# Optimization experiments

Measured on AMD Instinct MI355X. Metric: run time of the kernel, lower is better.

The kernel has to match this reference:

```python
import jax, jax.numpy as jnp
import numpy as np

B, L, S, H = 8, 128, 160, 768      # batch, words, wordpieces, bert hidden
T, CD = 16, 50                      # max chars per word, char embed/lstm dim
WV, WD = 50000, 100                 # word vocab, word embed dim
CV = 128                            # char vocab
NEG = -1e30


def _run_lstm(x, w_ih, w_hh, b):
    # x: [N, T, D] -> hidden states [N, T, Hc]; torch LSTM gate order i,f,g,o
    N = x.shape[0]
    Hc = w_hh.shape[1]
    def step(carry, xt):
        h, c = carry
        g = xt @ w_ih.T + h @ w_hh.T + b
        i, f, gg, o = jnp.split(g, 4, axis=-1)
        c = jax.nn.sigmoid(f) * c + jax.nn.sigmoid(i) * jnp.tanh(gg)
        h = jax.nn.sigmoid(o) * jnp.tanh(c)
        return (h, c), h
    init = (jnp.zeros((N, Hc), x.dtype), jnp.zeros((N, Hc), x.dtype))
    _, hs = jax.lax.scan(step, init, jnp.swapaxes(x, 0, 1))
    return jnp.swapaxes(hs, 0, 1)


def setup_inputs() -> dict:
    key = jax.random.key(0)
    ks = jax.random.split(key, 14)
    sc = 1.0 / np.sqrt(CD)
    return {
        "bert_emb": jax.random.normal(ks[0], (B, S, H), jnp.float32),
        "pieces2word": jax.random.randint(ks[1], (B, L, S), 0, 2, jnp.int32),
        "word_ids": jax.random.randint(ks[2], (B, L), 0, WV),
        "char_ids": jax.random.randint(ks[3], (B, L, T), 0, CV),
        "char_count": jax.random.randint(ks[4], (B, L), 0, T, jnp.int32),
        "token_masks_char": jax.random.randint(ks[5], (B, L, T), 0, 2, jnp.int32),
        "word_table": jax.random.normal(ks[6], (WV, WD), jnp.float32) * 0.02,
        "char_table": jax.random.normal(ks[7], (CV, CD), jnp.float32) * 0.02,
        "w_ih_f": jax.random.uniform(ks[8], (4 * CD, CD), jnp.float32, -sc, sc),
        "w_hh_f": jax.random.uniform(ks[9], (4 * CD, CD), jnp.float32, -sc, sc),
        "b_f": jax.random.uniform(ks[10], (4 * CD,), jnp.float32, -sc, sc),
        "w_ih_b": jax.random.uniform(ks[11], (4 * CD, CD), jnp.float32, -sc, sc),
        "w_hh_b": jax.random.uniform(ks[12], (4 * CD, CD), jnp.float32, -sc, sc),
        "b_b": jax.random.uniform(ks[13], (4 * CD,), jnp.float32, -sc, sc),
    }


def reference(bert_emb, pieces2word, word_ids, char_ids, char_count,
              token_masks_char, word_table, char_table,
              w_ih_f, w_hh_f, b_f, w_ih_b, w_hh_b, b_b):
    cls_embedding = bert_emb[:, 0]                      # [B, H]
    # piece -> word max pooling (masked fill with global min, then max)
    min_value = jax.lax.stop_gradient(jnp.min(bert_emb))
    expanded = jnp.where(pieces2word[:, :, :, None] != 0,
                         bert_emb[:, None, :, :], min_value)  # [B, L, S, H]
    word_reps = jnp.max(expanded, axis=2)               # [B, L, H]

    # word embedding lookup (emb_dropout is identity in eval)
    word_embed = word_table[word_ids]                   # [B, L, WD]

    # char biLSTM
    N = B * L
    lengths = jnp.maximum(char_count.reshape(N), 1)     # char_count[==0] = 1
    x = char_table[char_ids.reshape(N, T)]              # [N, T, CD]
    h_fwd = _run_lstm(x, w_ih_f, w_hh_f, b_f)           # [N, T, CD]
    # reverse each sequence by its true length (packed-sequence semantics)
    t = jnp.arange(T)
    rev_idx = lengths[:, None] - 1 - t[None, :]         # [N, T]
    valid = (rev_idx >= 0).astype(x.dtype)[:, :, None]
    gidx = jnp.clip(rev_idx, 0, T - 1)[:, :, None]
    x_rev = jnp.take_along_axis(x, gidx, axis=1) * valid
    h_rev = _run_lstm(x_rev, w_ih_b, w_hh_b, b_b)
    h_bwd = jnp.take_along_axis(h_rev, gidx, axis=1) * valid  # un-reverse + zero pad
    char_h = jnp.concatenate([h_fwd, h_bwd], axis=-1).reshape(B, L, T, 2 * CD)

    # combine(..., 'max'): additive -1e30 mask, max over chars, zero all-masked
    m = jnp.where(token_masks_char[:, :, :, None] == 0, NEG, 0.0).astype(char_h.dtype)
    h_token_char = jnp.max(m + char_h, axis=2)
    h_token_char = jnp.where(h_token_char == NEG, 0.0, h_token_char)  # [B, L, 2CD]

    embeds = jnp.concatenate([word_reps, word_embed, h_token_char], axis=-1)
    return embeds, cls_embedding
```

## Files before the change

kernel.cpp:

```cpp
#include <hip/hip_runtime.h>

#define B_   8
#define L_   128
#define S_   160
#define H_   768
#define T_   16
#define CD_  50
#define WD_  100
#define NGATE 200
#define NEGV (-1e30f)
#define FMAXV 3.402823466e+38f
#define NELEM (B_ * S_ * H_)

typedef short  s16x8 __attribute__((ext_vector_type(8)));
typedef float  f32x4 __attribute__((ext_vector_type(4)));

#define WL_OFF     0
#define WL_BYTES   (NGATE * 256)
#define XALL_OFF   (WL_OFF + WL_BYTES)
#define XALL_BYTES (T_ * 128 * 16)
#define HBUF_OFF   (XALL_OFF + XALL_BYTES)
#define HBUF_BYTES (2 * 128 * 16)
#define META_OFF   (HBUF_OFF + HBUF_BYTES)
#define SMEM_TOTAL (META_OFF + 32 * 4)

__device__ __forceinline__ unsigned short f2bf(float f) {
    unsigned u = __float_as_uint(f);
    u = (u + 0x7FFFu + ((u >> 16) & 1u)) >> 16;
    return (unsigned short)u;
}
__device__ __forceinline__ float sigm(float x) {
    return __fdividef(1.f, 1.f + __expf(-x));
}
__device__ __forceinline__ float tanh_fast(float x) {
    float a = fabsf(x);
    float e = __expf(-2.f * a);
    float t = __fdividef(1.f - e, 1.f + e);
    return copysignf(t, x);
}
__device__ __forceinline__ float4 fmax4(float4 a, float4 b) {
    return make_float4(fmaxf(a.x, b.x), fmaxf(a.y, b.y), fmaxf(a.z, b.z), fmaxf(a.w, b.w));
}

__device__ void lstm_body(int unit, char* smem,
        const int* __restrict__ char_ids, const int* __restrict__ char_count,
        const int* __restrict__ tok_mask, const float* __restrict__ char_table,
        const float* __restrict__ w_ih_f, const float* __restrict__ w_hh_f,
        const float* __restrict__ b_f,
        const float* __restrict__ w_ih_b, const float* __restrict__ w_hh_b,
        const float* __restrict__ b_b,
        float* __restrict__ out) {
    unsigned short* wl16 = (unsigned short*)(smem + WL_OFF);
    s16x8*          xal  = (s16x8*)(smem + XALL_OFF);
    s16x8*          hb   = (s16x8*)(smem + HBUF_OFF);
    int*            slen = (int*)(smem + META_OFF);
    int*            smask = slen + 16;

    const int dir  = unit >> 6;
    const int grp  = unit & 63;
    const int tid  = threadIdx.x;
    const int lane = tid & 63;
    const int wv   = tid >> 6;

    const float* WI = dir ? w_ih_b : w_ih_f;
    const float* WH = dir ? w_hh_b : w_hh_f;
    const float* BV = dir ? b_b    : b_f;

    if (tid < 16) {
        int n = grp * 16 + tid;
        int c = char_count[n];
        slen[tid] = (c > 0) ? c : 1;
        int mb = 0;
        for (int t = 0; t < T_; ++t) mb |= (tok_mask[n * T_ + t] != 0) << t;
        smask[tid] = mb;
    }
    if (tid < 256) { s16x8 z = {0,0,0,0,0,0,0,0}; hb[tid] = z; }

    for (int idx = tid; idx < NGATE * 16; idx += 512) {
        int r  = idx >> 4;
        int kc = idx & 15;
        int kbase = kc * 8;
        const float* wi = WI + r * CD_;
        const float* wh = WH + r * CD_;
        s16x8 fr = {0,0,0,0,0,0,0,0};
#pragma unroll
        for (int e = 0; e < 8; ++e) {
            int k = kbase + e;
            float v = 0.f;
            if (k < 64) {
                if (k < CD_) v = wi[k];
                else if (k == 63) v = BV[r];
            } else {
                int kk = k - 64;
                if (kk < CD_) v = wh[kk];
            }
            fr[e] = (short)f2bf(v);
        }
        *(s16x8*)((char*)wl16 + r * 256 + ((kc ^ (r & 7)) << 4)) = fr;
    }
    __syncthreads();

    for (int idx = tid; idx < T_ * 128; idx += 512) {
        int t = idx >> 7;
        int u = idx & 127;
        int g = u >> 4, s = u & 15;
        int st = dir ? (slen[s] - 1 - t) : t;
        s16x8 fr = {0,0,0,0,0,0,0,0};
        if (st >= 0) {
            int cidv = char_ids[(grp * 16 + s) * T_ + st];
            const float* row = char_table + cidv * CD_;
            int kbase = g * 8;
#pragma unroll
            for (int e = 0; e < 8; ++e) {
                int k = kbase + e;
                if (k < CD_) fr[e] = (short)f2bf(row[k]);
            }
        }
        if (g == 7) fr[7] = (short)0x3F80;
        xal[t * 128 + u] = fr;
    }

    const int m   = lane & 3;
    const int k2  = (lane >> 2) & 3;
    const int q   = lane >> 4;
    const int sstar = q * 4 + m;

    const int  ntA = wv;
    const int  ntB = 8 + wv;
    const bool hasB = (wv < 5);
    const int  cA = ntA * 4 + k2;
    const int  cB = ntB * 4 + k2;
    const bool vB = hasB && (cB < CD_);
    const int  hofsA = ((cA >> 3) * 16 + sstar) * 8 + (cA & 7);
    const int  hofsB = ((cB >> 3) * 16 + sstar) * 8 + (cB & 7);

    const int orowA = m * 50 + cA;
    const int orowB = m * 50 + ((cB < CD_) ? cB : 0);
#define WADDR(R, KT) ((R) * 256 + (((((KT) << 2) + q) ^ ((R) & 7)) << 4))
    const int baA0 = WADDR(orowA, 0), baA1 = WADDR(orowA, 1);
    const int baA2 = WADDR(orowA, 2), baA3 = WADDR(orowA, 3);
    const int baB0 = WADDR(orowB, 0), baB1 = WADDR(orowB, 1);
    const int baB2 = WADDR(orowB, 2), baB3 = WADDR(orowB, 3);

    const int laneofs = (q << 4) + (lane & 15);
    const int sl_s = slen[sstar];
    const int sm_s = smask[sstar];

    int sms = 0;
#pragma unroll
    for (int t = 0; t < T_; ++t) {
        int tt = dir ? (sl_s - 1 - t) : t;
        if (tt >= 0 && ((sm_s >> tt) & 1)) sms |= 1 << t;
    }

    float cstA = 0.f, cstB = 0.f;
    float mrA = NEGV, mrB = NEGV;
    const bool m0 = (lane & 1) != 0;
    const bool m1 = (lane & 2) != 0;

    __syncthreads();

    const char* wl = (const char*)wl16;

#define TRUPD(VLD, HOF, CST, MR, D) { \
    float v0 = (D)[0], v1 = (D)[1], v2 = (D)[2], v3 = (D)[3]; \
    float s10 = __shfl_xor(v0, 1), s11 = __shfl_xor(v1, 1); \
    float s12 = __shfl_xor(v2, 1), s13 = __shfl_xor(v3, 1); \
    float A0 = m0 ? s11 : v0; \
    float A1 = m0 ? v1 : s10; \
    float A2 = m0 ? s13 : v2; \
    float A3 = m0 ? v3 : s12; \
    float s20 = __shfl_xor(A0, 2), s21 = __shfl_xor(A1, 2); \
    float s22 = __shfl_xor(A2, 2), s23 = __shfl_xor(A3, 2); \
    float gi = m1 ? s22 : A0; \
    float gf = m1 ? s23 : A1; \
    float gg = m1 ? A2 : s20; \
    float go = m1 ? A3 : s21; \
    float cc = sigm(gf) * (CST) + sigm(gi) * tanh_fast(gg); \
    float h  = sigm(go) * tanh_fast(cc); \
    if (VLD) { \
        CST = cc; \
        hw[HOF] = f2bf(h); \
        if ((sms >> t) & 1) MR = fmaxf(MR, h); \
    } }

    __builtin_amdgcn_s_setprio(1);

#pragma unroll 1
    for (int t = 0; t < T_; ++t) {
        const int cur = t & 1, nxt = cur ^ 1;
        unsigned short* hw = (unsigned short*)(smem + HBUF_OFF) + nxt * 1024;
        const s16x8* xb = xal + t * 128;
        s16x8 a0 = xb[laneofs];
        s16x8 a1 = xb[64 + laneofs];
        s16x8 a2 = hb[cur * 128 + laneofs];
        s16x8 a3 = hb[cur * 128 + 64 + laneofs];

        {
            s16x8 w0 = *(const s16x8*)(wl + baA0);
            s16x8 w1 = *(const s16x8*)(wl + baA1);
            s16x8 w2 = *(const s16x8*)(wl + baA2);
            s16x8 w3 = *(const s16x8*)(wl + baA3);
            f32x4 d0 = {0.f, 0.f, 0.f, 0.f};
            d0 = __builtin_amdgcn_mfma_f32_16x16x32_bf16(a0, w0, d0, 0, 0, 0);
            d0 = __builtin_amdgcn_mfma_f32_16x16x32_bf16(a1, w1, d0, 0, 0, 0);
            d0 = __builtin_amdgcn_mfma_f32_16x16x32_bf16(a2, w2, d0, 0, 0, 0);
            d0 = __builtin_amdgcn_mfma_f32_16x16x32_bf16(a3, w3, d0, 0, 0, 0);
            TRUPD(true, hofsA, cstA, mrA, d0)
        }
        if (hasB) {
            s16x8 w0 = *(const s16x8*)(wl + baB0);
            s16x8 w1 = *(const s16x8*)(wl + baB1);
            s16x8 w2 = *(const s16x8*)(wl + baB2);
            s16x8 w3 = *(const s16x8*)(wl + baB3);
            f32x4 d1 = {0.f, 0.f, 0.f, 0.f};
            d1 = __builtin_amdgcn_mfma_f32_16x16x32_bf16(a0, w0, d1, 0, 0, 0);
            d1 = __builtin_amdgcn_mfma_f32_16x16x32_bf16(a1, w1, d1, 0, 0, 0);
            d1 = __builtin_amdgcn_mfma_f32_16x16x32_bf16(a2, w2, d1, 0, 0, 0);
            d1 = __builtin_amdgcn_mfma_f32_16x16x32_bf16(a3, w3, d1, 0, 0, 0);
            TRUPD(vB, hofsB, cstB, mrB, d1)
        }
        __syncthreads();
    }

    __builtin_amdgcn_s_setprio(0);

    float* ob = out + (size_t)(grp * 16 + sstar) * 968 + 868 + dir * CD_;
    {
        float mm = mrA;
        if (dir && (sm_s >> sl_s)) mm = fmaxf(mm, 0.f);
        if (mm == NEGV) mm = 0.f;
        ob[cA] = mm;
    }
    if (vB) {
        float mm = mrB;
        if (dir && (sm_s >> sl_s)) mm = fmaxf(mm, 0.f);
        if (mm == NEGV) mm = 0.f;
        ob[cB] = mm;
    }
}

struct Word2S {
    int   list[2][S_ + 8];
    int   cnt[2];
    float red[2][256];
};

__device__ void word_body2(int blk, char* smem,
        const float* __restrict__ bert, const int* __restrict__ p2w,
        const int* __restrict__ word_ids, const float* __restrict__ word_table,
        float* __restrict__ out) {
    Word2S& sh = *(Word2S*)smem;
    const int tid = threadIdx.x;
    const int h   = tid >> 8;
    const int lid = tid & 255;
    const int bl  = blk * 2 + h;
    const int b   = bl >> 7;
    const int l   = bl & 127;

    if (lid == 0) sh.cnt[h] = 0;
    __syncthreads();
    if (lid < S_) {
        if (p2w[bl * S_ + lid]) {
            int p = atomicAdd(&sh.cnt[h], 1);
            sh.list[h][p] = lid;
        }
    }
    __syncthreads();
    const int n = sh.cnt[h];
    if (n > 0 && lid < ((8 - (n & 7)) & 7)) sh.list[h][n + lid] = sh.list[h][0];
    __syncthreads();

    float gmin = 0.f;
    if (n == 0) {
        float mv = FMAXV;
        const float4* x4 = (const float4*)bert;
        for (int i = lid; i < NELEM / 4; i += 256) {
            float4 v = x4[i];
            mv = fminf(mv, fminf(fminf(v.x, v.y), fminf(v.z, v.w)));
        }
        sh.red[h][lid] = mv;
    }
    __syncthreads();
    if (n == 0) {
        float g = FMAXV;
        for (int k = 0; k < 256; ++k) g = fminf(g, sh.red[h][k]);
        gmin = g;
    }

    float* orow = out + (size_t)bl * 968;
    if (n > 0) {
        int n8 = (n + 7) & ~7;
        if (lid < 192) {
            const float4* bb = (const float4*)(bert + (size_t)b * S_ * H_) + lid;
            float4 mx = make_float4(-FMAXV, -FMAXV, -FMAXV, -FMAXV);
            const int* lst = sh.list[h];
            for (int i = 0; i < n8; i += 8) {
                float4 v0 = bb[(size_t)lst[i]     * 192];
                float4 v1 = bb[(size_t)lst[i + 1] * 192];
                float4 v2 = bb[(size_t)lst[i + 2] * 192];
                float4 v3 = bb[(size_t)lst[i + 3] * 192];
                float4 v4 = bb[(size_t)lst[i + 4] * 192];
                float4 v5 = bb[(size_t)lst[i + 5] * 192];
                float4 v6 = bb[(size_t)lst[i + 6] * 192];
                float4 v7 = bb[(size_t)lst[i + 7] * 192];
                mx = fmax4(mx, fmax4(fmax4(fmax4(v0, v1), fmax4(v2, v3)),
                                     fmax4(fmax4(v4, v5), fmax4(v6, v7))));
            }
            ((float4*)orow)[lid] = mx;
        } else {
            int j = lid - 192;
            int wid = word_ids[bl];
            orow[768 + j] = word_table[(size_t)wid * WD_ + j];
            if (j < WD_ - 64) orow[768 + 64 + j] = word_table[(size_t)wid * WD_ + 64 + j];
        }
    } else {
        if (lid < 192) {
            ((float4*)orow)[lid] = make_float4(gmin, gmin, gmin, gmin);
        } else {
            int j = lid - 192;
            int wid = word_ids[bl];
            orow[768 + j] = word_table[(size_t)wid * WD_ + j];
            if (j < WD_ - 64) orow[768 + 64 + j] = word_table[(size_t)wid * WD_ + 64 + j];
        }
    }

    if (l == 0 && lid < 192) {
        const float4* c4 = (const float4*)(bert + (size_t)b * S_ * H_);
        float4* co = (float4*)(out + (size_t)B_ * L_ * 968 + (size_t)b * H_);
        co[lid] = c4[lid];
    }
}

__global__ __launch_bounds__(512) void kmega(
        const float* __restrict__ bert, const int* __restrict__ p2w,
        const int* __restrict__ word_ids, const int* __restrict__ char_ids,
        const int* __restrict__ char_count, const int* __restrict__ tok_mask,
        const float* __restrict__ word_table, const float* __restrict__ char_table,
        const float* __restrict__ w_ih_f, const float* __restrict__ w_hh_f,
        const float* __restrict__ b_f,
        const float* __restrict__ w_ih_b, const float* __restrict__ w_hh_b,
        const float* __restrict__ b_b,
        float* __restrict__ out) {
    extern __shared__ __align__(16) char smem[];
    int bid = blockIdx.x;
    if (bid < 128) {
        lstm_body(bid, smem, char_ids, char_count, tok_mask, char_table,
                  w_ih_f, w_hh_f, b_f, w_ih_b, w_hh_b, b_b, out);
    } else {
        word_body2(bid - 128, smem, bert, p2w, word_ids, word_table, out);
    }
}

extern "C" void kernel_launch(void* const* d_in, const int* in_sizes, int n_in,
                              void* d_out, int out_size, void* d_ws, size_t ws_size,
                              hipStream_t stream) {
    const float* bert       = (const float*)d_in[0];
    const int*   p2w        = (const int*)d_in[1];
    const int*   word_ids   = (const int*)d_in[2];
    const int*   char_ids   = (const int*)d_in[3];
    const int*   char_count = (const int*)d_in[4];
    const int*   tok_mask   = (const int*)d_in[5];
    const float* word_table = (const float*)d_in[6];
    const float* char_table = (const float*)d_in[7];
    const float* w_ih_f = (const float*)d_in[8];
    const float* w_hh_f = (const float*)d_in[9];
    const float* b_f    = (const float*)d_in[10];
    const float* w_ih_b = (const float*)d_in[11];
    const float* w_hh_b = (const float*)d_in[12];
    const float* b_b    = (const float*)d_in[13];

    float* out = (float*)d_out;

    hipFuncSetAttribute((const void*)kmega,
                        hipFuncAttributeMaxDynamicSharedMemorySize, SMEM_TOTAL);

    kmega<<<128 + 512, 512, SMEM_TOTAL, stream>>>(bert, p2w, word_ids, char_ids, char_count,
                                                  tok_mask, word_table, char_table,
                                                  w_ih_f, w_hh_f, b_f, w_ih_b, w_hh_b, b_b, out);
}
```

Before: 42.16 us.

## Run each LSTM group in a single wave, removing per-step block barriers

The char-LSTM is restructured so that each wavefront independently handles one 16-word group and direction, computing all 13 gate tiles itself. Previously eight waves shared a group and synchronised with __syncthreads every timestep. The LSTM blocks shrink from 128 to 16. Character embeddings are now loaded straight from global memory one step ahead instead of being staged in LDS, and the MFMA operand order is swapped so the four gates land in one lane, with no shuffles. This removes per-step barriers and shuffle overhead, at the cost of a longer serial chain per wave and higher register pressure. A waves_per_eu hint is added.

```diff
diff --git a/kernel.cpp b/kernel.cpp
--- a/kernel.cpp
+++ b/kernel.cpp
@@ -15,14 +15,12 @@
 typedef short  s16x8 __attribute__((ext_vector_type(8)));
 typedef float  f32x4 __attribute__((ext_vector_type(4)));
 
-#define WL_OFF     0
 #define WL_BYTES   (NGATE * 256)
-#define XALL_OFF   (WL_OFF + WL_BYTES)
-#define XALL_BYTES (T_ * 128 * 16)
-#define HBUF_OFF   (XALL_OFF + XALL_BYTES)
-#define HBUF_BYTES (2 * 128 * 16)
-#define META_OFF   (HBUF_OFF + HBUF_BYTES)
-#define SMEM_TOTAL (META_OFF + 32 * 4)
+#define HB_OFF     WL_BYTES
+#define HB_BYTES   (8 * 2048)
+#define CID_OFF    (HB_OFF + HB_BYTES)
+#define CID_BYTES  (8 * 1024)
+#define SMEM_TOTAL (CID_OFF + CID_BYTES)
 
 __device__ __forceinline__ unsigned short f2bf(float f) {
     unsigned u = __float_as_uint(f);
@@ -42,7 +40,7 @@
     return make_float4(fmaxf(a.x, b.x), fmaxf(a.y, b.y), fmaxf(a.z, b.z), fmaxf(a.w, b.w));
 }
 
-__device__ void lstm_body(int unit, char* smem,
+__device__ void lstm_wave(int bid, char* smem,
         const int* __restrict__ char_ids, const int* __restrict__ char_count,
         const int* __restrict__ tok_mask, const float* __restrict__ char_table,
         const float* __restrict__ w_ih_f, const float* __restrict__ w_hh_f,
@@ -50,32 +48,18 @@
         const float* __restrict__ w_ih_b, const float* __restrict__ w_hh_b,
         const float* __restrict__ b_b,
         float* __restrict__ out) {
-    unsigned short* wl16 = (unsigned short*)(smem + WL_OFF);
-    s16x8*          xal  = (s16x8*)(smem + XALL_OFF);
-    s16x8*          hb   = (s16x8*)(smem + HBUF_OFF);
-    int*            slen = (int*)(smem + META_OFF);
-    int*            smask = slen + 16;
-
-    const int dir  = unit >> 6;
-    const int grp  = unit & 63;
     const int tid  = threadIdx.x;
     const int lane = tid & 63;
     const int wv   = tid >> 6;
-
-    const float* WI = dir ? w_ih_b : w_ih_f;
-    const float* WH = dir ? w_hh_b : w_hh_f;
-    const float* BV = dir ? b_b    : b_f;
-
-    if (tid < 16) {
-        int n = grp * 16 + tid;
-        int c = char_count[n];
-        slen[tid] = (c > 0) ? c : 1;
-        int mb = 0;
-        for (int t = 0; t < T_; ++t) mb |= (tok_mask[n * T_ + t] != 0) << t;
-        smask[tid] = mb;
-    }
-    if (tid < 256) { s16x8 z = {0,0,0,0,0,0,0,0}; hb[tid] = z; }
-
+    const int unit = bid * 8 + wv;
+    const int dirb = bid >> 3;
+    const int grp  = unit & 63;
+
+    const float* WI = dirb ? w_ih_b : w_ih_f;
+    const float* WH = dirb ? w_hh_b : w_hh_f;
+    const float* BV = dirb ? b_b    : b_f;
+
+    unsigned short* wl16 = (unsigned short*)smem;
     for (int idx = tid; idx < NGATE * 16; idx += 512) {
         int r  = idx >> 4;
         int kc = idx & 15;
@@ -98,146 +82,132 @@
         }
         *(s16x8*)((char*)wl16 + r * 256 + ((kc ^ (r & 7)) << 4)) = fr;
     }
-    __syncthreads();
-
-    for (int idx = tid; idx < T_ * 128; idx += 512) {
-        int t = idx >> 7;
-        int u = idx & 127;
-        int g = u >> 4, s = u & 15;
-        int st = dir ? (slen[s] - 1 - t) : t;
-        s16x8 fr = {0,0,0,0,0,0,0,0};
-        if (st >= 0) {
-            int cidv = char_ids[(grp * 16 + s) * T_ + st];
-            const float* row = char_table + cidv * CD_;
-            int kbase = g * 8;
+
+    int* cidW = (int*)(smem + CID_OFF) + wv * 256;
 #pragma unroll
-            for (int e = 0; e < 8; ++e) {
-                int k = kbase + e;
-                if (k < CD_) fr[e] = (short)f2bf(row[k]);
-            }
-        }
-        if (g == 7) fr[7] = (short)0x3F80;
-        xal[t * 128 + u] = fr;
-    }
-
-    const int m   = lane & 3;
-    const int k2  = (lane >> 2) & 3;
-    const int q   = lane >> 4;
-    const int sstar = q * 4 + m;
-
-    const int  ntA = wv;
-    const int  ntB = 8 + wv;
-    const bool hasB = (wv < 5);
-    const int  cA = ntA * 4 + k2;
-    const int  cB = ntB * 4 + k2;
-    const bool vB = hasB && (cB < CD_);
-    const int  hofsA = ((cA >> 3) * 16 + sstar) * 8 + (cA & 7);
-    const int  hofsB = ((cB >> 3) * 16 + sstar) * 8 + (cB & 7);
-
-    const int orowA = m * 50 + cA;
-    const int orowB = m * 50 + ((cB < CD_) ? cB : 0);
-#define WADDR(R, KT) ((R) * 256 + (((((KT) << 2) + q) ^ ((R) & 7)) << 4))
-    const int baA0 = WADDR(orowA, 0), baA1 = WADDR(orowA, 1);
-    const int baA2 = WADDR(orowA, 2), baA3 = WADDR(orowA, 3);
-    const int baB0 = WADDR(orowB, 0), baB1 = WADDR(orowB, 1);
-    const int baB2 = WADDR(orowB, 2), baB3 = WADDR(orowB, 3);
-
-    const int laneofs = (q << 4) + (lane & 15);
-    const int sl_s = slen[sstar];
-    const int sm_s = smask[sstar];
-
+    for (int j = 0; j < 4; ++j) {
+        int idx = lane * 4 + j;
+        int ss = idx >> 4, t2 = idx & 15;
+        cidW[idx] = char_ids[(grp * 16 + ss) * T_ + t2];
+    }
+    char* hbS = smem + HB_OFF + wv * 2048;
+    { s16x8 z = {0,0,0,0,0,0,0,0};
+      *(s16x8*)(hbS + lane * 16) = z;
+      *(s16x8*)(hbS + (64 + lane) * 16) = z; }
+
+    __syncthreads();
+
+    const int s  = lane & 15;
+    const int q  = lane >> 4;
+    const int m  = lane & 3;
+    const int k2 = (lane >> 2) & 3;
+    const int base_row = m * 50 + k2;
+
+    const int n = grp * 16 + s;
+    int c = char_count[n];
+    const int sl_s = (c > 0) ? c : 1;
+    int sm_s = 0;
+#pragma unroll
+    for (int t2 = 0; t2 < T_; ++t2) sm_s |= (tok_mask[n * T_ + t2] != 0) << t2;
     int sms = 0;
 #pragma unroll
-    for (int t = 0; t < T_; ++t) {
-        int tt = dir ? (sl_s - 1 - t) : t;
-        if (tt >= 0 && ((sm_s >> tt) & 1)) sms |= 1 << t;
-    }
-
-    float cstA = 0.f, cstB = 0.f;
-    float mrA = NEGV, mrB = NEGV;
-    const bool m0 = (lane & 1) != 0;
-    const bool m1 = (lane & 2) != 0;
-
-    __syncthreads();
+    for (int t2 = 0; t2 < T_; ++t2) {
+        int tt = dirb ? (sl_s - 1 - t2) : t2;
+        if (tt >= 0 && ((sm_s >> tt) & 1)) sms |= 1 << t2;
+    }
 
     const char* wl = (const char*)wl16;
-
-#define TRUPD(VLD, HOF, CST, MR, D) { \
-    float v0 = (D)[0], v1 = (D)[1], v2 = (D)[2], v3 = (D)[3]; \
-    float s10 = __shfl_xor(v0, 1), s11 = __shfl_xor(v1, 1); \
-    float s12 = __shfl_xor(v2, 1), s13 = __shfl_xor(v3, 1); \
-    float A0 = m0 ? s11 : v0; \
-    float A1 = m0 ? v1 : s10; \
-    float A2 = m0 ? s13 : v2; \
-    float A3 = m0 ? v3 : s12; \
-    float s20 = __shfl_xor(A0, 2), s21 = __shfl_xor(A1, 2); \
-    float s22 = __shfl_xor(A2, 2), s23 = __shfl_xor(A3, 2); \
-    float gi = m1 ? s22 : A0; \
-    float gf = m1 ? s23 : A1; \
-    float gg = m1 ? A2 : s20; \
-    float go = m1 ? A3 : s21; \
-    float cc = sigm(gf) * (CST) + sigm(gi) * tanh_fast(gg); \
-    float h  = sigm(go) * tanh_fast(cc); \
-    if (VLD) { \
+    unsigned short* hwS = (unsigned short*)hbS;
+
+#define XLOAD(PX0, PX1, ST) { \
+    _Pragma("unroll") for (int e = 0; e < 8; ++e) { PX0[e] = 0.f; PX1[e] = 0.f; } \
+    if ((ST) >= 0) { \
+        int cidv = cidW[s * 16 + (ST)]; \
+        const float* row = char_table + cidv * CD_; \
+        _Pragma("unroll") for (int e = 0; e < 8; ++e) PX0[e] = row[q * 8 + e]; \
+        _Pragma("unroll") for (int e = 0; e < 8; ++e) { \
+            int k = 32 + q * 8 + e; if (k < CD_) PX1[e] = row[k]; } \
+    } }
+#define XPACK(A0, A1, PX0, PX1) { \
+    s16x8 t0_, t1_; \
+    _Pragma("unroll") for (int e = 0; e < 8; ++e) { \
+        t0_[e] = (short)f2bf(PX0[e]); t1_[e] = (short)f2bf(PX1[e]); } \
+    if (q == 3) t1_[7] = (short)0x3F80;     \
+    A0 = t0_; A1 = t1_; }
+
+#define TILE(NT, CST, MR) { \
+    int R_ = base_row + 4 * (NT); \
+    R_ = (R_ < NGATE) ? R_ : (NGATE - 1);         \
+    const int sw_ = R_ & 7; \
+    const char* wr_ = wl + R_ * 256; \
+    s16x8 w0 = *(const s16x8*)(wr_ + (((0  + q) ^ sw_) << 4)); \
+    s16x8 w1 = *(const s16x8*)(wr_ + (((4  + q) ^ sw_) << 4)); \
+    s16x8 w2 = *(const s16x8*)(wr_ + (((8  + q) ^ sw_) << 4)); \
+    s16x8 w3 = *(const s16x8*)(wr_ + (((12 + q) ^ sw_) << 4)); \
+    f32x4 d = {0.f, 0.f, 0.f, 0.f}; \
+    d = __builtin_amdgcn_mfma_f32_16x16x32_bf16(w0, a0, d, 0, 0, 0); \
+    d = __builtin_amdgcn_mfma_f32_16x16x32_bf16(w1, a1, d, 0, 0, 0); \
+    d = __builtin_amdgcn_mfma_f32_16x16x32_bf16(w2, a2h, d, 0, 0, 0); \
+    d = __builtin_amdgcn_mfma_f32_16x16x32_bf16(w3, a3h, d, 0, 0, 0); \
+    const int cell_ = (NT) * 4 + q; \
+    float cc = sigm(d[1]) * (CST) + sigm(d[0]) * tanh_fast(d[2]); \
+    float h  = sigm(d[3]) * tanh_fast(cc); \
+    if (cell_ < CD_) { \
         CST = cc; \
-        hw[HOF] = f2bf(h); \
+        hwS[((cell_ >> 3) * 16 + s) * 8 + (cell_ & 7)] = f2bf(h); \
         if ((sms >> t) & 1) MR = fmaxf(MR, h); \
     } }
 
+    float cst0=0.f,cst1=0.f,cst2=0.f,cst3=0.f,cst4=0.f,cst5=0.f,cst6=0.f,
+          cst7=0.f,cst8=0.f,cst9=0.f,cst10=0.f,cst11=0.f,cst12=0.f;
+    float mr0=NEGV,mr1=NEGV,mr2=NEGV,mr3=NEGV,mr4=NEGV,mr5=NEGV,mr6=NEGV,
+          mr7=NEGV,mr8=NEGV,mr9=NEGV,mr10=NEGV,mr11=NEGV,mr12=NEGV;
+
+    s16x8 a0, a1;
+    {
+        float px0[8], px1[8];
+        int st0 = dirb ? (sl_s - 1) : 0;
+        XLOAD(px0, px1, st0)
+        XPACK(a0, a1, px0, px1)
+    }
+    asm volatile("" ::: "memory");
+
     __builtin_amdgcn_s_setprio(1);
 
 #pragma unroll 1
     for (int t = 0; t < T_; ++t) {
-        const int cur = t & 1, nxt = cur ^ 1;
-        unsigned short* hw = (unsigned short*)(smem + HBUF_OFF) + nxt * 1024;
-        const s16x8* xb = xal + t * 128;
-        s16x8 a0 = xb[laneofs];
-        s16x8 a1 = xb[64 + laneofs];
-        s16x8 a2 = hb[cur * 128 + laneofs];
-        s16x8 a3 = hb[cur * 128 + 64 + laneofs];
-
-        {
-            s16x8 w0 = *(const s16x8*)(wl + baA0);
-            s16x8 w1 = *(const s16x8*)(wl + baA1);
-            s16x8 w2 = *(const s16x8*)(wl + baA2);
-            s16x8 w3 = *(const s16x8*)(wl + baA3);
-            f32x4 d0 = {0.f, 0.f, 0.f, 0.f};
-            d0 = __builtin_amdgcn_mfma_f32_16x16x32_bf16(a0, w0, d0, 0, 0, 0);
-            d0 = __builtin_amdgcn_mfma_f32_16x16x32_bf16(a1, w1, d0, 0, 0, 0);
-            d0 = __builtin_amdgcn_mfma_f32_16x16x32_bf16(a2, w2, d0, 0, 0, 0);
-            d0 = __builtin_amdgcn_mfma_f32_16x16x32_bf16(a3, w3, d0, 0, 0, 0);
-            TRUPD(true, hofsA, cstA, mrA, d0)
-        }
-        if (hasB) {
-            s16x8 w0 = *(const s16x8*)(wl + baB0);
-            s16x8 w1 = *(const s16x8*)(wl + baB1);
-            s16x8 w2 = *(const s16x8*)(wl + baB2);
-            s16x8 w3 = *(const s16x8*)(wl + baB3);
-            f32x4 d1 = {0.f, 0.f, 0.f, 0.f};
-            d1 = __builtin_amdgcn_mfma_f32_16x16x32_bf16(a0, w0, d1, 0, 0, 0);
-            d1 = __builtin_amdgcn_mfma_f32_16x16x32_bf16(a1, w1, d1, 0, 0, 0);
-            d1 = __builtin_amdgcn_mfma_f32_16x16x32_bf16(a2, w2, d1, 0, 0, 0);
-            d1 = __builtin_amdgcn_mfma_f32_16x16x32_bf16(a3, w3, d1, 0, 0, 0);
-            TRUPD(vB, hofsB, cstB, mrB, d1)
-        }
-        __syncthreads();
+        float px0[8], px1[8];
+        int st1 = (t + 1 < T_) ? (dirb ? (sl_s - 1 - (t + 1)) : (t + 1)) : -1;
+        XLOAD(px0, px1, st1)
+
+        s16x8 a2h = *(const s16x8*)(hbS + (q * 16 + s) * 16);
+        s16x8 a3h = *(const s16x8*)(hbS + ((q + 4) * 16 + s) * 16);
+
+        TILE(0,  cst0,  mr0)  TILE(1,  cst1,  mr1)  TILE(2,  cst2,  mr2)
+        TILE(3,  cst3,  mr3)  TILE(4,  cst4,  mr4)  TILE(5,  cst5,  mr5)
+        TILE(6,  cst6,  mr6)  TILE(7,  cst7,  mr7)  TILE(8,  cst8,  mr8)
+        TILE(9,  cst9,  mr9)  TILE(10, cst10, mr10) TILE(11, cst11, mr11)
+        TILE(12, cst12, mr12)
+
+        XPACK(a0, a1, px0, px1)
+        asm volatile("" ::: "memory");
     }
 
     __builtin_amdgcn_s_setprio(0);
 
-    float* ob = out + (size_t)(grp * 16 + sstar) * 968 + 868 + dir * CD_;
-    {
-        float mm = mrA;
-        if (dir && (sm_s >> sl_s)) mm = fmaxf(mm, 0.f);
-        if (mm == NEGV) mm = 0.f;
-        ob[cA] = mm;
-    }
-    if (vB) {
-        float mm = mrB;
-        if (dir && (sm_s >> sl_s)) mm = fmaxf(mm, 0.f);
-        if (mm == NEGV) mm = 0.f;
-        ob[cB] = mm;
-    }
+    float* ob = out + (size_t)(grp * 16 + s) * 968 + 868 + dirb * CD_;
+#define OUTC(NT, MR) { \
+    const int cell_ = (NT) * 4 + q; \
+    if (cell_ < CD_) { \
+        float mm = MR; \
+        if (dirb && (sm_s >> sl_s)) mm = fmaxf(mm, 0.f); \
+        if (mm == NEGV) mm = 0.f; \
+        ob[cell_] = mm; \
+    } }
+    OUTC(0,  mr0)  OUTC(1,  mr1)  OUTC(2,  mr2)  OUTC(3,  mr3)
+    OUTC(4,  mr4)  OUTC(5,  mr5)  OUTC(6,  mr6)  OUTC(7,  mr7)
+    OUTC(8,  mr8)  OUTC(9,  mr9)  OUTC(10, mr10) OUTC(11, mr11)
+    OUTC(12, mr12)
 }
 
 struct Word2S {
@@ -332,7 +302,9 @@
     }
 }
 
-__global__ __launch_bounds__(512) void kmega(
+__global__ __launch_bounds__(512)
+__attribute__((amdgpu_waves_per_eu(2, 4)))
+void kmega(
         const float* __restrict__ bert, const int* __restrict__ p2w,
         const int* __restrict__ word_ids, const int* __restrict__ char_ids,
         const int* __restrict__ char_count, const int* __restrict__ tok_mask,
@@ -344,11 +316,11 @@
         float* __restrict__ out) {
     extern __shared__ __align__(16) char smem[];
     int bid = blockIdx.x;
-    if (bid < 128) {
-        lstm_body(bid, smem, char_ids, char_count, tok_mask, char_table,
+    if (bid < 16) {
+        lstm_wave(bid, smem, char_ids, char_count, tok_mask, char_table,
                   w_ih_f, w_hh_f, b_f, w_ih_b, w_hh_b, b_b, out);
     } else {
-        word_body2(bid - 128, smem, bert, p2w, word_ids, word_table, out);
+        word_body2(bid - 16, smem, bert, p2w, word_ids, word_table, out);
     }
 }
 
@@ -375,7 +347,7 @@
     hipFuncSetAttribute((const void*)kmega,
                         hipFuncAttributeMaxDynamicSharedMemorySize, SMEM_TOTAL);
 
-    kmega<<<128 + 512, 512, SMEM_TOTAL, stream>>>(bert, p2w, word_ids, char_ids, char_count,
-                                                  tok_mask, word_table, char_table,
-                                                  w_ih_f, w_hh_f, b_f, w_ih_b, w_hh_b, b_b, out);
-}
+    kmega<<<16 + 512, 512, SMEM_TOTAL, stream>>>(bert, p2w, word_ids, char_ids, char_count,
+                                                 tok_mask, word_table, char_table,
+                                                 w_ih_f, w_hh_f, b_f, w_ih_b, w_hh_b, b_b, out);
+}
```

After: 109.3 us. 159% more time.
